# Performance work log

Measured on AMD Instinct MI355X. Metric: run time of the kernel, lower is better.

## Reference

```python
import jax, jax.numpy as jnp
import numpy as np

B, N, D = 32, 128, 1024


def _euclid_cost(a, b):
    # a: [N, D], b: [N, D] -> [N, N] Euclidean distances (torch.cdist p=2)
    a = a.astype(np.float64)
    b = b.astype(np.float64)
    sq = (a * a).sum(-1)[:, None] + (b * b).sum(-1)[None, :] - 2.0 * (a @ b.T)
    return np.sqrt(np.maximum(sq, 0.0))


def _hungarian(cost):
    """Exact LAP via shortest augmenting path (Kuhn-Munkres with potentials).
    Returns col_for_row: row i is matched to column col_for_row[i].
    Equivalent to scipy.optimize.linear_sum_assignment on a square matrix
    (row_ind == arange(N))."""
    n = cost.shape[0]
    INF = 1e18
    c = cost.astype(np.float64)
    u = np.zeros(n + 1)
    v = np.zeros(n + 1)
    p = np.zeros(n + 1, dtype=np.int64)   # p[j] = row matched to column j (1-based)
    way = np.zeros(n + 1, dtype=np.int64)
    for i in range(1, n + 1):
        p[0] = i
        j0 = 0
        minv = np.full(n + 1, INF)
        used = np.zeros(n + 1, dtype=bool)
        while True:
            used[j0] = True
            i0 = p[j0]
            free = ~used[1:]
            cand = c[i0 - 1] - u[i0] - v[1:]
            better = free & (cand < minv[1:])
            idx = np.nonzero(better)[0]
            minv[idx + 1] = cand[idx]
            way[idx + 1] = j0
            free_j = np.nonzero(free)[0] + 1
            j1 = free_j[np.argmin(minv[free_j])]
            delta = minv[j1]
            u[p[used]] += delta
            v[used] -= delta
            minv[~used] -= delta
            j0 = j1
            if p[j0] == 0:
                break
        while j0:
            j1 = way[j0]
            p[j0] = p[j1]
            j0 = j1
    col_for_row = np.zeros(n, dtype=np.int64)
    for j in range(1, n + 1):
        col_for_row[p[j] - 1] = j - 1
    return col_for_row


def _match(pred_nodes, target_nodes):
    # Host-side exact bipartite matching (mirrors the .cpu() + scipy solve;
    # non-differentiable, indices treated as constants like torch's detach()).
    pn = np.asarray(jax.device_get(pred_nodes))
    tn = np.asarray(jax.device_get(target_nodes))
    cols = [_hungarian(_euclid_cost(pn[b], tn[b])) for b in range(pn.shape[0])]
    return jnp.asarray(np.stack(cols))  # [B, N] int64


def setup_inputs() -> dict:
    key = jax.random.key(0)
    k1, k2, k3, k4 = jax.random.split(key, 4)
    return {
        "pred_nodes": jax.random.normal(k1, (B, N, D), dtype=jnp.float32),
        "target_nodes": jax.random.normal(k2, (B, N, D), dtype=jnp.float32),
        "pred_adj": jax.random.normal(k3, (B, N, N), dtype=jnp.float32),
        "target_adj": jax.random.normal(k4, (B, N, N), dtype=jnp.float32),
    }


def reference(pred_nodes, target_nodes, pred_adj, target_adj):
    col = _match(pred_nodes, target_nodes)  # [B, N]; row_ind is identity
    # matched target nodes: target_nodes[b][col_ind]
    tn_m = jnp.take_along_axis(target_nodes, col[:, :, None], axis=1)  # [B, N, D]
    # nn.MSELoss() = mean over elements per sample; losses summed over batch
    node_loss = jnp.mean((pred_nodes - tn_m) ** 2, axis=(1, 2)).sum()
    # target_adj[b][col_ind][:, col_ind]; pred_adj row_ind gather is identity
    ta_m = jnp.take_along_axis(target_adj, col[:, :, None], axis=1)
    ta_m = jnp.take_along_axis(ta_m, col[:, None, :], axis=2)  # [B, N, N]
    edge_loss = jnp.mean((pred_adj - ta_m) ** 2, axis=(1, 2)).sum()
    return node_loss, edge_loss
```

## Files before the change

### kernel.cpp

```cpp
#include <hip/hip_runtime.h>
#include <hip/hip_bf16.h>
#include <math.h>

#define BB 32
#define NN 128
#define DD 1024
#define INF64 1e30

__global__ __launch_bounds__(128) void cost_kernel(const float* __restrict__ pred,
                                                   const float* __restrict__ tgt,
                                                   double* __restrict__ cost) {
  int blk = blockIdx.x;
  int b = blk >> 4;
  int it = (blk & 15) << 3;
  const float* Ab = pred + ((size_t)b * NN + it) * DD;
  const float* Bb = tgt + (size_t)b * NN * DD;
  __shared__ float a_s[8 * DD];
  for (int t = threadIdx.x; t < 8 * DD / 4; t += 128) {
    ((float4*)a_s)[t] = ((const float4*)Ab)[t];
  }
  __syncthreads();
  const int j = threadIdx.x;
  const float4* brow = (const float4*)(Bb + (size_t)j * DD);
  double acc[8];
#pragma unroll
  for (int r = 0; r < 8; r++) acc[r] = 0.0;
  for (int k4 = 0; k4 < DD / 4; k4++) {
    float4 bv = brow[k4];
#pragma unroll
    for (int r = 0; r < 8; r++) {
      float4 av = ((const float4*)(a_s + r * DD))[k4];
      double d0 = (double)av.x - (double)bv.x;
      double d1 = (double)av.y - (double)bv.y;
      double d2 = (double)av.z - (double)bv.z;
      double d3 = (double)av.w - (double)bv.w;
      acc[r] += d0 * d0 + d1 * d1 + d2 * d2 + d3 * d3;
    }
  }
#pragma unroll
  for (int r = 0; r < 8; r++) {
    cost[(((size_t)b * NN) + it + r) * NN + j] = sqrt(acc[r]);
  }
}

union f64u { double d; unsigned int i[2]; };

__device__ __forceinline__ double readlane_f64(double x, int lane) {
  f64u u; u.d = x;
  f64u v;
  v.i[0] = (unsigned)__builtin_amdgcn_readlane((int)u.i[0], lane);
  v.i[1] = (unsigned)__builtin_amdgcn_readlane((int)u.i[1], lane);
  return v.d;
}

__device__ __forceinline__ double readpair_f64(double a, double b, int idx) {
  int l = (idx - 1) & 63;
  double ra = readlane_f64(a, l);
  double rb = readlane_f64(b, l);
  return ((idx - 1) >> 6) ? rb : ra;
}

__device__ __forceinline__ int readpair_i32(int a, int b, int idx) {
  int l = (idx - 1) & 63;
  int ra = __builtin_amdgcn_readlane(a, l);
  int rb = __builtin_amdgcn_readlane(b, l);
  return ((idx - 1) >> 6) ? rb : ra;
}

__device__ __forceinline__ double pack_key(double m, int idx) {
  unsigned long long bits = __double_as_longlong(fmax(m, 0.0));
  bits = (bits & ~127ull) | (unsigned long long)idx;
  return __longlong_as_double(bits);
}

#define DPP_MIN_STEP(r, CTRL)                                                        \
  do {                                                                               \
    f64u _t; _t.d = (r);                                                             \
    f64u _s;                                                                         \
    _s.i[0] = (unsigned)__builtin_amdgcn_update_dpp((int)_t.i[0], (int)_t.i[0],      \
                                                    (CTRL), 0xF, 0xF, false);        \
    _s.i[1] = (unsigned)__builtin_amdgcn_update_dpp((int)_t.i[1], (int)_t.i[1],      \
                                                    (CTRL), 0xF, 0xF, false);        \
    (r) = fmin((r), _s.d);                                                           \
  } while (0)

__global__ __launch_bounds__(64) void hungarian_kernel(const double* __restrict__ cost,
                                                       int* __restrict__ colfor) {
  extern __shared__ double lds[];
  const int b = blockIdx.x;
  const double* C = cost + (size_t)b * NN * NN;
  const int lane = threadIdx.x;
  const int jA = lane + 1;
  const int jB = lane + 65;

  {
    const double2* src = (const double2*)C;
    double2* dst = (double2*)lds;
#pragma unroll 8
    for (int t = lane; t < NN * NN / 2; t += 64) dst[t] = src[t];
  }
  __syncthreads();

  double vA = INF64, vB = INF64;
  int argA = 0, argB = 0;
#pragma unroll 4
  for (int i = 0; i < NN; i++) {
    double cA = lds[(size_t)i * NN + lane];
    double cB = lds[(size_t)i * NN + lane + 64];
    if (cA < vA) { vA = cA; argA = i + 1; }
    if (cB < vB) { vB = cB; argB = i + 1; }
  }

  unsigned long long asgLo = 0ull, asgHi = 0ull;
  int pA = 0, pB = 0;
  for (int j = 1; j <= NN; j++) {
    int ar = readpair_i32(argA, argB, j);
    bool freeRow = (ar <= 64) ? !((asgLo >> (ar - 1)) & 1ull)
                              : !((asgHi >> (ar - 65)) & 1ull);
    if (freeRow) {
      if (ar <= 64) asgLo |= 1ull << (ar - 1); else asgHi |= 1ull << (ar - 65);
      if (j == jA) pA = ar;
      if (j == jB) pB = ar;
    }
  }

  double uA = 0.0, uB = 0.0;

  for (int i = 1; i <= NN; i++) {
    bool seeded = (i <= 64) ? ((asgLo >> (i - 1)) & 1ull)
                            : ((asgHi >> (i - 65)) & 1ull);
    if (seeded) continue;

    double minvA = INF64, minvB = INF64;
    int wayA = 0, wayB = 0;
    int usedA = 0, usedB = 0;
    unsigned long long usedRowLo = 0ull, usedRowHi = 0ull;
    int j0 = 0;
    int i0 = i;
    int jfin;
    while (true) {
      usedA |= (j0 == jA);
      usedB |= (j0 == jB);
      if (i0 <= 64) usedRowLo |= 1ull << (i0 - 1); else usedRowHi |= 1ull << (i0 - 65);
      double u_i0 = readpair_f64(uA, uB, i0);
      const double* crow = lds + (size_t)(i0 - 1) * NN;
      double cA = crow[lane];
      double cB = crow[lane + 64];
      double candA = cA - u_i0 - vA;
      double candB = cB - u_i0 - vB;
      if (!usedA && candA < minvA) { minvA = candA; wayA = j0; }
      if (!usedB && candB < minvB) { minvB = candB; wayB = j0; }
      double kA = pack_key(usedA ? INF64 : minvA, lane);
      double kB = pack_key(usedB ? INF64 : minvB, lane + 64);
      double r = fmin(kA, kB);
      DPP_MIN_STEP(r, 0x111);
      DPP_MIN_STEP(r, 0x112);
      DPP_MIN_STEP(r, 0x114);
      DPP_MIN_STEP(r, 0x118);
      DPP_MIN_STEP(r, 0x142);
      DPP_MIN_STEP(r, 0x143);
      double rmin = readlane_f64(r, 63);
      unsigned long long bits = __double_as_longlong(rmin);
      int j1 = (int)(bits & 127ull) + 1;
      double delta = __longlong_as_double(bits & ~127ull);
      if ((usedRowLo >> lane) & 1ull) uA += delta;
      if ((usedRowHi >> lane) & 1ull) uB += delta;
      if (usedA) vA -= delta; else minvA -= delta;
      if (usedB) vB -= delta; else minvB -= delta;
      int pj1 = readpair_i32(pA, pB, j1);
      j0 = j1;
      if (pj1 == 0) { jfin = j1; break; }
      i0 = pj1;
    }
    int j = jfin;
    while (j) {
      int wj = readpair_i32(wayA, wayB, j);
      int pn = (wj == 0) ? i : readpair_i32(pA, pB, wj);
      if (j == jA) pA = pn;
      if (j == jB) pB = pn;
      j = wj;
    }
  }
  colfor[b * NN + (pA - 1)] = jA - 1;
  colfor[b * NN + (pB - 1)] = jB - 1;
}

__global__ __launch_bounds__(256) void node_loss_kernel(const float* __restrict__ pred,
                                                        const float* __restrict__ tgt,
                                                        const int* __restrict__ col,
                                                        double* __restrict__ partial) {
  const size_t total = (size_t)BB * NN * (DD / 4);
  double s = 0.0;
  for (size_t idx = (size_t)blockIdx.x * blockDim.x + threadIdx.x; idx < total;
       idx += (size_t)gridDim.x * blockDim.x) {
    size_t k4 = idx & (DD / 4 - 1);
    size_t bi = idx / (DD / 4);
    int i = (int)(bi & (NN - 1));
    int b = (int)(bi >> 7);
    int c = col[b * NN + i];
    float4 pv = ((const float4*)pred)[idx];
    float4 tv = ((const float4*)(tgt + ((size_t)b * NN + c) * DD))[k4];
    float d0 = pv.x - tv.x, d1 = pv.y - tv.y, d2 = pv.z - tv.z, d3 = pv.w - tv.w;
    s += (double)d0 * d0 + (double)d1 * d1 + (double)d2 * d2 + (double)d3 * d3;
  }
  __shared__ double red[256];
  red[threadIdx.x] = s;
  __syncthreads();
  for (int off = 128; off > 0; off >>= 1) {
    if (threadIdx.x < off) red[threadIdx.x] += red[threadIdx.x + off];
    __syncthreads();
  }
  if (threadIdx.x == 0) partial[blockIdx.x] = red[0];
}

__global__ __launch_bounds__(256) void edge_loss_kernel(const float* __restrict__ padj,
                                                        const float* __restrict__ tadj,
                                                        const int* __restrict__ col,
                                                        double* __restrict__ partial) {
  const size_t total = (size_t)BB * NN * NN;
  double s = 0.0;
  for (size_t idx = (size_t)blockIdx.x * blockDim.x + threadIdx.x; idx < total;
       idx += (size_t)gridDim.x * blockDim.x) {
    int j = (int)(idx & (NN - 1));
    size_t bi = idx >> 7;
    int i = (int)(bi & (NN - 1));
    int b = (int)(bi >> 7);
    int ci = col[b * NN + i];
    int cj = col[b * NN + j];
    float diff = padj[idx] - tadj[((size_t)b * NN + ci) * NN + cj];
    s += (double)diff * (double)diff;
  }
  __shared__ double red[256];
  red[threadIdx.x] = s;
  __syncthreads();
  for (int off = 128; off > 0; off >>= 1) {
    if (threadIdx.x < off) red[threadIdx.x] += red[threadIdx.x + off];
    __syncthreads();
  }
  if (threadIdx.x == 0) partial[blockIdx.x] = red[0];
}

__global__ __launch_bounds__(256) void finalize_kernel(const double* __restrict__ nodeP, int nNode,
                                                       const double* __restrict__ edgeP, int nEdge,
                                                       float* __restrict__ out) {
  __shared__ double red[256];
  double s = 0.0;
  for (int t = threadIdx.x; t < nNode; t += 256) s += nodeP[t];
  red[threadIdx.x] = s;
  __syncthreads();
  for (int off = 128; off > 0; off >>= 1) {
    if (threadIdx.x < off) red[threadIdx.x] += red[threadIdx.x + off];
    __syncthreads();
  }
  double nodeSum = red[0];
  __syncthreads();
  s = 0.0;
  for (int t = threadIdx.x; t < nEdge; t += 256) s += edgeP[t];
  red[threadIdx.x] = s;
  __syncthreads();
  for (int off = 128; off > 0; off >>= 1) {
    if (threadIdx.x < off) red[threadIdx.x] += red[threadIdx.x + off];
    __syncthreads();
  }
  if (threadIdx.x == 0) {
    out[0] = (float)(nodeSum / (double)(NN * DD));
    out[1] = (float)(red[0] / (double)(NN * NN));
  }
}

extern "C" void kernel_launch(void* const* d_in, const int* in_sizes, int n_in,
                              void* d_out, int out_size, void* d_ws, size_t ws_size,
                              hipStream_t stream) {
  const float* pred_nodes   = (const float*)d_in[0];
  const float* target_nodes = (const float*)d_in[1];
  const float* pred_adj     = (const float*)d_in[2];
  const float* target_adj   = (const float*)d_in[3];
  float* out = (float*)d_out;

  char* ws = (char*)d_ws;
  double* cost = (double*)ws;
  size_t off = (size_t)BB * NN * NN * sizeof(double);
  int* col = (int*)(ws + off);
  off += (size_t)BB * NN * sizeof(int);
  double* nodeP = (double*)(ws + off);
  double* edgeP = nodeP + 512;

  cost_kernel<<<BB * 16, 128, 0, stream>>>(pred_nodes, target_nodes, cost);
  hungarian_kernel<<<BB, 64, 131072, stream>>>(cost, col);
  node_loss_kernel<<<512, 256, 0, stream>>>(pred_nodes, target_nodes, col, nodeP);
  edge_loss_kernel<<<128, 256, 0, stream>>>(pred_adj, target_adj, col, edgeP);
  finalize_kernel<<<1, 256, 0, stream>>>(nodeP, 512, edgeP, 128, out);
}
```

Measured before the change: 831.9 us.

## Use norm-expansion cost, interleaved LDS layout, and bitmask free-column tracking

The cost kernel now computes squared distances as |a|^2 + |b|^2 - 2a·b, with A rows pre-converted to double in a 64 KB dynamic LDS buffer. This removes the per-element float-to-double conversions and subtractions but changes rounding and doubles the A tile's LDS footprint, which can cut occupancy. The Hungarian kernel stores cost rows as interleaved double2 pairs so each lane needs one 16-byte LDS load per row. It also iterates unseeded rows through a bitmask and tests whether a column is free via a ballot bitmask instead of a cross-lane readlane.

```diff
diff --git a/kernel.cpp b/kernel.cpp
--- a/kernel.cpp
+++ b/kernel.cpp
@@ -10,14 +10,30 @@
 __global__ __launch_bounds__(128) void cost_kernel(const float* __restrict__ pred,
                                                    const float* __restrict__ tgt,
                                                    double* __restrict__ cost) {
+  extern __shared__ double a_s[];
+  __shared__ double na_s[8];
   int blk = blockIdx.x;
   int b = blk >> 4;
   int it = (blk & 15) << 3;
   const float* Ab = pred + ((size_t)b * NN + it) * DD;
   const float* Bb = tgt + (size_t)b * NN * DD;
-  __shared__ float a_s[8 * DD];
   for (int t = threadIdx.x; t < 8 * DD / 4; t += 128) {
-    ((float4*)a_s)[t] = ((const float4*)Ab)[t];
+    float4 v = ((const float4*)Ab)[t];
+    double2* d = (double2*)&a_s[(size_t)t * 4];
+    d[0] = double2{(double)v.x, (double)v.y};
+    d[1] = double2{(double)v.z, (double)v.w};
+  }
+  __syncthreads();
+  if (threadIdx.x < 8) {
+    const double* ar = a_s + (size_t)threadIdx.x * DD;
+    double s0 = 0, s1 = 0, s2 = 0, s3 = 0;
+    for (int k = 0; k < DD; k += 4) {
+      s0 += ar[k] * ar[k];
+      s1 += ar[k + 1] * ar[k + 1];
+      s2 += ar[k + 2] * ar[k + 2];
+      s3 += ar[k + 3] * ar[k + 3];
+    }
+    na_s[threadIdx.x] = (s0 + s1) + (s2 + s3);
   }
   __syncthreads();
   const int j = threadIdx.x;
@@ -25,21 +41,22 @@
   double acc[8];
 #pragma unroll
   for (int r = 0; r < 8; r++) acc[r] = 0.0;
+  double nb = 0.0;
   for (int k4 = 0; k4 < DD / 4; k4++) {
     float4 bv = brow[k4];
+    double b0 = (double)bv.x, b1 = (double)bv.y, b2 = (double)bv.z, b3 = (double)bv.w;
+    nb += b0 * b0 + b1 * b1 + b2 * b2 + b3 * b3;
+    const double* ar = a_s + (size_t)k4 * 4;
 #pragma unroll
     for (int r = 0; r < 8; r++) {
-      float4 av = ((const float4*)(a_s + r * DD))[k4];
-      double d0 = (double)av.x - (double)bv.x;
-      double d1 = (double)av.y - (double)bv.y;
-      double d2 = (double)av.z - (double)bv.z;
-      double d3 = (double)av.w - (double)bv.w;
-      acc[r] += d0 * d0 + d1 * d1 + d2 * d2 + d3 * d3;
+      const double* a = ar + (size_t)r * DD;
+      acc[r] += a[0] * b0 + a[1] * b1 + a[2] * b2 + a[3] * b3;
     }
   }
 #pragma unroll
   for (int r = 0; r < 8; r++) {
-    cost[(((size_t)b * NN) + it + r) * NN + j] = sqrt(acc[r]);
+    double sq = na_s[r] + nb - 2.0 * acc[r];
+    cost[(((size_t)b * NN) + it + r) * NN + j] = sqrt(fmax(sq, 0.0));
   }
 }
 
@@ -84,6 +101,16 @@
     (r) = fmin((r), _s.d);                                                           \
   } while (0)
 
+#define DPP_MIN_CHAIN(r)          \
+  do {                            \
+    DPP_MIN_STEP(r, 0x111);       \
+    DPP_MIN_STEP(r, 0x112);       \
+    DPP_MIN_STEP(r, 0x114);       \
+    DPP_MIN_STEP(r, 0x118);       \
+    DPP_MIN_STEP(r, 0x142);       \
+    DPP_MIN_STEP(r, 0x143);       \
+  } while (0)
+
 __global__ __launch_bounds__(64) void hungarian_kernel(const double* __restrict__ cost,
                                                        int* __restrict__ colfor) {
   extern __shared__ double lds[];
@@ -94,10 +121,13 @@
   const int jB = lane + 65;
 
   {
-    const double2* src = (const double2*)C;
     double2* dst = (double2*)lds;
-#pragma unroll 8
-    for (int t = lane; t < NN * NN / 2; t += 64) dst[t] = src[t];
+#pragma unroll 4
+    for (int i = 0; i < NN; i++) {
+      double gA = C[(size_t)i * NN + lane];
+      double gB = C[(size_t)i * NN + lane + 64];
+      dst[i * 64 + lane] = double2{gA, gB};
+    }
   }
   __syncthreads();
 
@@ -105,10 +135,9 @@
   int argA = 0, argB = 0;
 #pragma unroll 4
   for (int i = 0; i < NN; i++) {
-    double cA = lds[(size_t)i * NN + lane];
-    double cB = lds[(size_t)i * NN + lane + 64];
-    if (cA < vA) { vA = cA; argA = i + 1; }
-    if (cB < vB) { vB = cB; argB = i + 1; }
+    double2 cc = ((const double2*)lds)[i * 64 + lane];
+    if (cc.x < vA) { vA = cc.x; argA = i + 1; }
+    if (cc.y < vB) { vB = cc.y; argB = i + 1; }
   }
 
   unsigned long long asgLo = 0ull, asgHi = 0ull;
@@ -124,12 +153,15 @@
     }
   }
 
+  unsigned long long freeLo = __ballot(pA == 0);
+  unsigned long long freeHi = __ballot(pB == 0);
+
   double uA = 0.0, uB = 0.0;
-
-  for (int i = 1; i <= NN; i++) {
-    bool seeded = (i <= 64) ? ((asgLo >> (i - 1)) & 1ull)
-                            : ((asgHi >> (i - 65)) & 1ull);
-    if (seeded) continue;
+  unsigned long long mLo = ~asgLo, mHi = ~asgHi;
+
+  while ((mLo | mHi) != 0ull) {
+    int i = mLo ? (__builtin_ctzll(mLo) + 1) : (__builtin_ctzll(mHi) + 65);
+    if (i <= 64) mLo &= ~(1ull << (i - 1)); else mHi &= ~(1ull << (i - 65));
 
     double minvA = INF64, minvB = INF64;
     int wayA = 0, wayB = 0;
@@ -137,41 +169,35 @@
     unsigned long long usedRowLo = 0ull, usedRowHi = 0ull;
     int j0 = 0;
     int i0 = i;
-    int jfin;
     while (true) {
       usedA |= (j0 == jA);
       usedB |= (j0 == jB);
       if (i0 <= 64) usedRowLo |= 1ull << (i0 - 1); else usedRowHi |= 1ull << (i0 - 65);
       double u_i0 = readpair_f64(uA, uB, i0);
-      const double* crow = lds + (size_t)(i0 - 1) * NN;
-      double cA = crow[lane];
-      double cB = crow[lane + 64];
-      double candA = cA - u_i0 - vA;
-      double candB = cB - u_i0 - vB;
+      double2 cc = ((const double2*)lds)[(i0 - 1) * 64 + lane];
+      double candA = cc.x - u_i0 - vA;
+      double candB = cc.y - u_i0 - vB;
       if (!usedA && candA < minvA) { minvA = candA; wayA = j0; }
       if (!usedB && candB < minvB) { minvB = candB; wayB = j0; }
       double kA = pack_key(usedA ? INF64 : minvA, lane);
       double kB = pack_key(usedB ? INF64 : minvB, lane + 64);
       double r = fmin(kA, kB);
-      DPP_MIN_STEP(r, 0x111);
-      DPP_MIN_STEP(r, 0x112);
-      DPP_MIN_STEP(r, 0x114);
-      DPP_MIN_STEP(r, 0x118);
-      DPP_MIN_STEP(r, 0x142);
-      DPP_MIN_STEP(r, 0x143);
+      DPP_MIN_CHAIN(r);
       double rmin = readlane_f64(r, 63);
       unsigned long long bits = __double_as_longlong(rmin);
       int j1 = (int)(bits & 127ull) + 1;
-      double delta = __longlong_as_double(bits & ~127ull);
+      double delta = __longlong_as_double((long long)(bits & ~127ull));
       if ((usedRowLo >> lane) & 1ull) uA += delta;
       if ((usedRowHi >> lane) & 1ull) uB += delta;
       if (usedA) vA -= delta; else minvA -= delta;
       if (usedB) vB -= delta; else minvB -= delta;
-      int pj1 = readpair_i32(pA, pB, j1);
+      bool isFree = (j1 <= 64) ? ((freeLo >> (j1 - 1)) & 1ull)
+                               : ((freeHi >> (j1 - 65)) & 1ull);
       j0 = j1;
-      if (pj1 == 0) { jfin = j1; break; }
-      i0 = pj1;
-    }
+      if (isFree) break;
+      i0 = readpair_i32(pA, pB, j1);
+    }
+    int jfin = j0;
     int j = jfin;
     while (j) {
       int wj = readpair_i32(wayA, wayB, j);
@@ -180,6 +206,8 @@
       if (j == jB) pB = pn;
       j = wj;
     }
+    if (jfin <= 64) freeLo &= ~(1ull << (jfin - 1));
+    else            freeHi &= ~(1ull << (jfin - 65));
   }
   colfor[b * NN + (pA - 1)] = jA - 1;
   colfor[b * NN + (pB - 1)] = jB - 1;
@@ -285,7 +313,7 @@
   double* nodeP = (double*)(ws + off);
   double* edgeP = nodeP + 512;
 
-  cost_kernel<<<BB * 16, 128, 0, stream>>>(pred_nodes, target_nodes, cost);
+  cost_kernel<<<BB * 16, 128, 65536, stream>>>(pred_nodes, target_nodes, cost);
   hungarian_kernel<<<BB, 64, 131072, stream>>>(cost, col);
   node_loss_kernel<<<512, 256, 0, stream>>>(pred_nodes, target_nodes, col, nodeP);
   edge_loss_kernel<<<128, 256, 0, stream>>>(pred_adj, target_adj, col, edgeP);
```

New measurement: 946.8 us. +13.8%, slower.
